# Performance work log

Measured on AMD Instinct MI355X. Metric: run time of the kernel, lower is better.

Reference implementation:

```python
import jax, jax.numpy as jnp
import numpy as np

B, S, D = 4, 4096, 2048
DQ = D // 4          # router hidden
DF = 4 * D           # layer_fn FFN hidden
CAPACITY = 0.125


def setup_inputs() -> dict:
    key = jax.random.key(0)
    ks = jax.random.split(key, 5)
    sc = 0.02
    return {
        "x":   jax.random.normal(ks[0], (B, S, D), jnp.float32),
        "Wr1": jax.random.normal(ks[1], (D, DQ), jnp.float32) * sc,
        "br1": jnp.zeros((DQ,), jnp.float32),
        "Wr2": jax.random.normal(ks[2], (DQ, 1), jnp.float32) * sc,
        "br2": jnp.zeros((1,), jnp.float32),
        "Wf1": jax.random.normal(ks[3], (D, DF), jnp.float32) * sc,
        "bf1": jnp.zeros((DF,), jnp.float32),
        "Wf2": jax.random.normal(ks[4], (DF, D), jnp.float32) * sc,
        "bf2": jnp.zeros((D,), jnp.float32),
    }


def reference(x, Wr1, br1, Wr2, br2, Wf1, bf1, Wf2, bf2):
    b, s, d = x.shape
    k = max(1, int(CAPACITY * s))

    # router: Linear -> ReLU -> Linear -> squeeze(-1)
    h = jax.nn.relu(jnp.einsum("bsd,dq->bsq", x, Wr1) + br1)
    scores = (jnp.einsum("bsq,qo->bso", h, Wr2) + br2)[..., 0]   # [B, S]

    # top-k token selection per batch row
    topk_scores, topk_idx = jax.lax.top_k(scores, k)             # [B, k]

    # gather selected tokens
    sel = jnp.take_along_axis(x, topk_idx[..., None], axis=1)    # [B, k, D]

    # layer_fn: standard FFN (D -> 4D -> D) on selected tokens only
    proc = jnp.einsum("bkf,fd->bkd",
                      jax.nn.relu(jnp.einsum("bkd,df->bkf", sel, Wf1) + bf1),
                      Wf2) + bf2                                 # [B, k, D]

    # scatter processed tokens back into a copy of x
    batch_idx = jnp.arange(b)[:, None]                           # [B, 1]
    output = x.at[batch_idx, topk_idx].set(proc)                 # [B, S, D]

    mask = jnp.zeros((b, s), dtype=bool).at[batch_idx, topk_idx].set(True)
    return output, mask
```

## Files before the change

kernel.cpp:

```cpp
#include <hip/hip_runtime.h>

#define B_    4
#define S_    4096
#define D_    2048
#define DQ_   512
#define DF_   8192
#define KSEL_ 512
#define M_    (B_ * S_)
#define MS_   (B_ * KSEL_)

typedef __attribute__((ext_vector_type(8))) short bf16x8;
typedef __attribute__((ext_vector_type(4))) float f32x4;
typedef __attribute__((address_space(3))) void as3_void;
typedef const __attribute__((address_space(1))) void as1_cvoid;

__device__ __forceinline__ unsigned short f2bf(float f) {
    unsigned u = __float_as_uint(f);
    u += 0x7FFFu + ((u >> 16) & 1u);
    return (unsigned short)(u >> 16);
}
__device__ __forceinline__ float bf2f(unsigned short h) {
    return __uint_as_float(((unsigned)h) << 16);
}

__device__ __forceinline__ void gload16(const void* g, void* l) {
    __builtin_amdgcn_global_load_lds((as1_cvoid*)g, (as3_void*)l, 16, 0, 0);
}

__global__ void split_copy_kernel(const float* __restrict__ x,
                                  unsigned short* __restrict__ xh,
                                  unsigned short* __restrict__ xl,
                                  float* __restrict__ out, int n8) {
    int i = blockIdx.x * blockDim.x + threadIdx.x;
    int stride = gridDim.x * blockDim.x;
    for (; i < n8; i += stride) {
        float4 a = ((const float4*)x)[2 * i];
        float4 b = ((const float4*)x)[2 * i + 1];
        ((float4*)out)[2 * i]     = a;
        ((float4*)out)[2 * i + 1] = b;
        float v[8] = {a.x, a.y, a.z, a.w, b.x, b.y, b.z, b.w};
        unsigned short hi[8], lo[8];
#pragma unroll
        for (int j = 0; j < 8; j++) {
            hi[j] = f2bf(v[j]);
            lo[j] = f2bf(v[j] - bf2f(hi[j]));
        }
        *(uint4*)(xh + (size_t)i * 8) = *(const uint4*)hi;
        *(uint4*)(xl + (size_t)i * 8) = *(const uint4*)lo;
    }
}

__global__ void wsplit_kernel(const float* __restrict__ W,
                              unsigned short* __restrict__ whiT,
                              unsigned short* __restrict__ wloT) {
    __shared__ float tile[32][33];
    int tx = threadIdx.x, ty = threadIdx.y;
    int n0 = blockIdx.x * 32, k0 = blockIdx.y * 32;
#pragma unroll
    for (int j = 0; j < 4; j++)
        tile[ty + j * 8][tx] = W[(size_t)(k0 + ty + j * 8) * DQ_ + n0 + tx];
    __syncthreads();
#pragma unroll
    for (int j = 0; j < 4; j++) {
        float v = tile[tx][ty + j * 8];
        unsigned short hi = f2bf(v);
        unsigned short lo = f2bf(v - bf2f(hi));
        size_t row = (size_t)(n0 + ty + j * 8) * D_;
        whiT[row + k0 + tx] = hi;
        wloT[row + k0 + tx] = lo;
    }
}

__global__ void transpose_bf16_kernel(const float* __restrict__ in,
                                      unsigned short* __restrict__ out,
                                      int R, int C) {
    __shared__ float tile[32][33];
    int tx = threadIdx.x, ty = threadIdx.y;
    int c0 = blockIdx.x * 32, r0 = blockIdx.y * 32;
#pragma unroll
    for (int j = 0; j < 4; j++)
        tile[ty + j * 8][tx] = in[(size_t)(r0 + ty + j * 8) * C + c0 + tx];
    __syncthreads();
#pragma unroll
    for (int j = 0; j < 4; j++)
        out[(size_t)(c0 + ty + j * 8) * R + r0 + tx] = f2bf(tile[tx][ty + j * 8]);
}

#define RSTAGE(bufp, ktX) do {                                              \
    const size_t ko_ = (size_t)(ktX) * 32;                                  \
    char* laH_ = (char*)(&sA[bufp][0][0]) + w * 1024;                       \
    char* laL_ = (char*)(&sA[bufp][1][0]) + w * 1024;                       \
    char* lbH_ = (char*)(&sB[bufp][0][0]) + w * 1024;                       \
    char* lbL_ = (char*)(&sB[bufp][1][0]) + w * 1024;                       \
    gload16(gAh + ko_,            laH_);                                    \
    gload16(gAh + 64 * D_ + ko_,  laH_ + 4096);                             \
    gload16(gAl + ko_,            laL_);                                    \
    gload16(gAl + 64 * D_ + ko_,  laL_ + 4096);                             \
    gload16(gBh + ko_,            lbH_);                                    \
    gload16(gBh + 64 * D_ + ko_,  lbH_ + 4096);                             \
    gload16(gBl + ko_,            lbL_);                                    \
    gload16(gBl + 64 * D_ + ko_,  lbL_ + 4096);                             \
  } while (0)

__global__ __launch_bounds__(256) void router_mfma(const unsigned short* __restrict__ xh,
                                                   const unsigned short* __restrict__ xl,
                                                   const unsigned short* __restrict__ whiT,
                                                   const unsigned short* __restrict__ wloT,
                                                   const float* __restrict__ br1,
                                                   const float* __restrict__ Wr2,
                                                   float* __restrict__ pscore) {
    __shared__ unsigned short sA[2][2][128 * 32];
    __shared__ unsigned short sB[2][2][128 * 32];
    const int t = threadIdx.x;
    const int w = t >> 6, l = t & 63;
    const int m0 = blockIdx.x * 128, n0 = blockIdx.y * 128;
    const int wr = w >> 1, wc = w & 1;

    f32x4 acc[4][4];
    const f32x4 zz = {0.f, 0.f, 0.f, 0.f};
#pragma unroll
    for (int m = 0; m < 4; m++)
#pragma unroll
        for (int n = 0; n < 4; n++) acc[m][n] = zz;

    const int srow = t >> 2;
    const int sch8 = (((t & 3) ^ ((t >> 3) & 3)) * 8);
    const unsigned short* gAh = xh + (size_t)(m0 + srow) * D_ + sch8;
    const unsigned short* gAl = xl + (size_t)(m0 + srow) * D_ + sch8;
    const unsigned short* gBh = whiT + (size_t)(n0 + srow) * D_ + sch8;
    const unsigned short* gBl = wloT + (size_t)(n0 + srow) * D_ + sch8;

    RSTAGE(0, 0);
    RSTAGE(1, 1);

    const int fro = ((l >> 4) ^ ((l >> 1) & 3)) * 8;
    const int arB = (wr * 64 + (l & 15)) * 32 + fro;
    const int brB = (wc * 64 + (l & 15)) * 32 + fro;

    for (int kt = 0; kt < 64; ++kt) {
        if (kt + 1 < 64) { asm volatile("s_waitcnt vmcnt(8)" ::: "memory"); }
        else             { asm volatile("s_waitcnt vmcnt(0)" ::: "memory"); }
        __builtin_amdgcn_s_barrier();
        __builtin_amdgcn_sched_barrier(0);
        const int cur = kt & 1;
        const unsigned short* LAh = &sA[cur][0][0];
        const unsigned short* LAl = &sA[cur][1][0];
        const unsigned short* LBh = &sB[cur][0][0];
        const unsigned short* LBl = &sB[cur][1][0];
        bf16x8 ah[4], al[4], bh[4], bl[4];
#pragma unroll
        for (int f = 0; f < 4; f++) ah[f] = *(const bf16x8*)(LAh + arB + f * 512);
#pragma unroll
        for (int f = 0; f < 4; f++) bh[f] = *(const bf16x8*)(LBh + brB + f * 512);
#pragma unroll
        for (int f = 0; f < 4; f++) bl[f] = *(const bf16x8*)(LBl + brB + f * 512);
#pragma unroll
        for (int f = 0; f < 4; f++) al[f] = *(const bf16x8*)(LAl + arB + f * 512);
        __builtin_amdgcn_s_setprio(1);
#pragma unroll
        for (int m = 0; m < 4; m++)
#pragma unroll
            for (int n = 0; n < 4; n++)
                acc[m][n] = __builtin_amdgcn_mfma_f32_16x16x32_bf16(ah[m], bh[n], acc[m][n], 0, 0, 0);
#pragma unroll
        for (int m = 0; m < 4; m++)
#pragma unroll
            for (int n = 0; n < 4; n++)
                acc[m][n] = __builtin_amdgcn_mfma_f32_16x16x32_bf16(ah[m], bl[n], acc[m][n], 0, 0, 0);
#pragma unroll
        for (int m = 0; m < 4; m++)
#pragma unroll
            for (int n = 0; n < 4; n++)
                acc[m][n] = __builtin_amdgcn_mfma_f32_16x16x32_bf16(al[m], bh[n], acc[m][n], 0, 0, 0);
        __builtin_amdgcn_s_setprio(0);
        __builtin_amdgcn_sched_barrier(0);
        __builtin_amdgcn_s_barrier();
        if (kt + 2 < 64) RSTAGE(cur, kt + 2);
    }

    float br1v[4], wr2v[4];
#pragma unroll
    for (int nf = 0; nf < 4; nf++) {
        int col = n0 + wc * 64 + nf * 16 + (l & 15);
        br1v[nf] = br1[col];
        wr2v[nf] = Wr2[col];
    }
#pragma unroll
    for (int mf = 0; mf < 4; mf++)
#pragma unroll
        for (int q = 0; q < 4; q++) {
            float s = 0.f;
#pragma unroll
            for (int nf = 0; nf < 4; nf++)
                s += fmaxf(acc[mf][nf][q] + br1v[nf], 0.f) * wr2v[nf];
#pragma unroll
            for (int off = 8; off >= 1; off >>= 1)
                s += __shfl_xor(s, off);
            if ((l & 15) == 0) {
                int row = m0 + wr * 64 + mf * 16 + (l >> 4) * 4 + q;
                pscore[(size_t)(blockIdx.y * 2 + wc) * M_ + row] = s;
            }
        }
}

__global__ __launch_bounds__(1024) void topk_kernel(const float* __restrict__ pscore,
                                                    const float* __restrict__ br2,
                                                    int* __restrict__ sel_idx,
                                                    float* __restrict__ maskF) {
    __shared__ unsigned long long keys[S_];
    __shared__ unsigned char flags[S_];
    int b = blockIdx.x, t = threadIdx.x;
    float bb = br2[0];
    for (int i = t; i < S_; i += 1024) {
        int m = b * S_ + i;
        float f = bb;
#pragma unroll
        for (int s8 = 0; s8 < 8; s8++) f += pscore[(size_t)s8 * M_ + m];
        unsigned u = __float_as_uint(f);
        u = (u & 0x80000000u) ? ~u : (u | 0x80000000u);
        keys[i] = ((unsigned long long)u << 32) | (unsigned)(S_ - 1 - i);
        flags[i] = 0;
    }
    __syncthreads();
    for (int k = 2; k <= S_; k <<= 1)
        for (int j = k >> 1; j > 0; j >>= 1) {
            for (int i = t; i < S_; i += 1024) {
                int l = i ^ j;
                if (l > i) {
                    unsigned long long a = keys[i], c = keys[l];
                    bool up = ((i & k) == 0);
                    if (up ? (a > c) : (a < c)) { keys[i] = c; keys[l] = a; }
                }
            }
            __syncthreads();
        }
    for (int i = t; i < KSEL_; i += 1024) {
        unsigned long long kk = keys[S_ - KSEL_ + i];
        int s = (S_ - 1) - (int)(kk & 0xFFFFFFFFu);
        sel_idx[b * KSEL_ + i] = s;
        flags[s] = 1;
    }
    __syncthreads();
    for (int i = t; i < S_; i += 1024)
        maskF[b * S_ + i] = flags[i] ? 1.0f : 0.0f;
}

__global__ void gather_kernel(const float* __restrict__ x, const int* __restrict__ sel_idx,
                              unsigned short* __restrict__ sel) {
    int jrow = blockIdx.x;
    int b = jrow >> 9;
    int tok = sel_idx[jrow];
    const float* src = x + ((size_t)(b * S_ + tok)) * D_;
    int t = threadIdx.x;
    float4 v0 = ((const float4*)src)[2 * t];
    float4 v1 = ((const float4*)src)[2 * t + 1];
    unsigned p0 = (unsigned)f2bf(v0.x) | ((unsigned)f2bf(v0.y) << 16);
    unsigned p1 = (unsigned)f2bf(v0.z) | ((unsigned)f2bf(v0.w) << 16);
    unsigned p2 = (unsigned)f2bf(v1.x) | ((unsigned)f2bf(v1.y) << 16);
    unsigned p3 = (unsigned)f2bf(v1.z) | ((unsigned)f2bf(v1.w) << 16);
    *(uint4*)(sel + (size_t)jrow * D_ + t * 8) = make_uint4(p0, p1, p2, p3);
}

#define STAGEAB(bufp, ktX) do {                                                   \
    const unsigned short* a_ = gA + (size_t)(ktX) * 64;                           \
    const unsigned short* b_ = gB + (size_t)(ktX) * 64;                           \
    char* la_ = (char*)(&lds[bufp][0][0]) + w * 1024;                             \
    char* lb_ = (char*)(&lds[bufp][1][0]) + w * 1024;                             \
    gload16(a_,                      la_);                                        \
    gload16(a_ +  64 * (size_t)K,    la_ + 8192);                                 \
    gload16(a_ + 128 * (size_t)K,    la_ + 16384);                                \
    gload16(a_ + 192 * (size_t)K,    la_ + 24576);                                \
    gload16(b_,                      lb_);                                        \
    gload16(b_ +  64 * (size_t)K,    lb_ + 8192);                                 \
    gload16(b_ + 128 * (size_t)K,    lb_ + 16384);                                \
    gload16(b_ + 192 * (size_t)K,    lb_ + 24576);                                \
  } while (0)

__global__ __launch_bounds__(512) void mfma_gemm256(const unsigned short* __restrict__ A,
                                                    const unsigned short* __restrict__ Bt,
                                                    int M, int N, int K, int kspan,
                                                    const float* __restrict__ bias,
                                                    unsigned short* __restrict__ Cbf,
                                                    float* __restrict__ partial,
                                                    int epi) {
    __shared__ unsigned short lds[2][2][256 * 64];
    const int t = threadIdx.x;
    const int w = t >> 6, l = t & 63;
    const int m0 = blockIdx.y * 256, n0 = blockIdx.x * 256;
    const int wr = w >> 2, wc = w & 3;
    const int kbeg = blockIdx.z * kspan;
    const int NT = kspan / 64;

    f32x4 acc[8][4];
    const f32x4 zz = {0.f, 0.f, 0.f, 0.f};
#pragma unroll
    for (int m = 0; m < 8; m++)
#pragma unroll
        for (int n = 0; n < 4; n++) acc[m][n] = zz;

    const int srow = t >> 3;
    const int sch8 = (((t & 7) ^ ((t >> 3) & 7)) * 8);
    const unsigned short* gA = A + (size_t)(m0 + srow) * K + kbeg + sch8;
    const unsigned short* gB = Bt + (size_t)(n0 + srow) * K + kbeg + sch8;

    STAGEAB(0, 0);
    STAGEAB(1, 1);

    for (int kt = 0; kt < NT; ++kt) {
        if (kt + 1 < NT) { asm volatile("s_waitcnt vmcnt(8)" ::: "memory"); }
        else             { asm volatile("s_waitcnt vmcnt(0)" ::: "memory"); }
        __builtin_amdgcn_s_barrier();
        __builtin_amdgcn_sched_barrier(0);
        const int cur = kt & 1;
        const unsigned short* LA = &lds[cur][0][0];
        const unsigned short* LB = &lds[cur][1][0];
#pragma unroll
        for (int kk = 0; kk < 2; kk++) {
            const int sw_ = ((kk * 4 + (l >> 4)) ^ (l & 7)) * 8;
            bf16x8 bfr[4], af0[4], af1[4];
#pragma unroll
            for (int n = 0; n < 4; n++)
                bfr[n] = *(const bf16x8*)(LB + (wc * 64 + n * 16 + (l & 15)) * 64 + sw_);
#pragma unroll
            for (int m = 0; m < 4; m++) {
                af0[m] = *(const bf16x8*)(LA + (wr * 128 + m * 16 + (l & 15)) * 64 + sw_);
                af1[m] = *(const bf16x8*)(LA + (wr * 128 + 64 + m * 16 + (l & 15)) * 64 + sw_);
            }
            __builtin_amdgcn_s_setprio(1);
#pragma unroll
            for (int m = 0; m < 4; m++)
#pragma unroll
                for (int n = 0; n < 4; n++)
                    acc[m][n] = __builtin_amdgcn_mfma_f32_16x16x32_bf16(af0[m], bfr[n], acc[m][n], 0, 0, 0);
#pragma unroll
            for (int m = 0; m < 4; m++)
#pragma unroll
                for (int n = 0; n < 4; n++)
                    acc[4 + m][n] = __builtin_amdgcn_mfma_f32_16x16x32_bf16(af1[m], bfr[n], acc[4 + m][n], 0, 0, 0);
            __builtin_amdgcn_s_setprio(0);
        }
        __builtin_amdgcn_sched_barrier(0);
        __builtin_amdgcn_s_barrier();
        if (kt + 2 < NT) STAGEAB(cur, kt + 2);
    }

    if (epi == 0) {
#pragma unroll
        for (int m = 0; m < 8; m++) {
            int rowb = m0 + wr * 128 + m * 16 + (l >> 4) * 4;
#pragma unroll
            for (int n = 0; n < 4; n++) {
                int col = n0 + wc * 64 + n * 16 + (l & 15);
                float bv = bias[col];
#pragma unroll
                for (int q = 0; q < 4; q++) {
                    float v = fmaxf(acc[m][n][q] + bv, 0.f);
                    Cbf[(size_t)(rowb + q) * N + col] = f2bf(v);
                }
            }
        }
    } else {
        float* pseg = partial + (size_t)blockIdx.z * M * N;
#pragma unroll
        for (int m = 0; m < 8; m++) {
            int rowb = m0 + wr * 128 + m * 16 + (l >> 4) * 4;
#pragma unroll
            for (int n = 0; n < 4; n++) {
                int col = n0 + wc * 64 + n * 16 + (l & 15);
#pragma unroll
                for (int q = 0; q < 4; q++)
                    pseg[(size_t)(rowb + q) * N + col] = acc[m][n][q];
            }
        }
    }
}

__global__ void reduce_scatter_kernel(const float* __restrict__ partial,
                                      const float* __restrict__ bias,
                                      const int* __restrict__ sel_idx,
                                      float* __restrict__ out) {
    int m = blockIdx.x;
    int t = threadIdx.x;
    int brow = m >> 9;
    int tok = sel_idx[m];
    float* orow = out + ((size_t)(brow * S_ + tok)) * D_;
    const float* p0 = partial + (size_t)m * D_;
    const size_t seg = (size_t)MS_ * D_;
#pragma unroll
    for (int r = 0; r < 2; r++) {
        int c = (t + r * 256) * 4;
        float4 v0 = *(const float4*)(p0 + c);
        float4 v1 = *(const float4*)(p0 + seg + c);
        float4 v2 = *(const float4*)(p0 + 2 * seg + c);
        float4 v3 = *(const float4*)(p0 + 3 * seg + c);
        float4 bv = *(const float4*)(bias + c);
        float4 o;
        o.x = v0.x + v1.x + v2.x + v3.x + bv.x;
        o.y = v0.y + v1.y + v2.y + v3.y + bv.y;
        o.z = v0.z + v1.z + v2.z + v3.z + bv.z;
        o.w = v0.w + v1.w + v2.w + v3.w + bv.w;
        *(float4*)(orow + c) = o;
    }
}

extern "C" void kernel_launch(void* const* d_in, const int* in_sizes, int n_in,
                              void* d_out, int out_size, void* d_ws, size_t ws_size,
                              hipStream_t stream) {
    const float* x   = (const float*)d_in[0];
    const float* Wr1 = (const float*)d_in[1];
    const float* br1 = (const float*)d_in[2];
    const float* Wr2 = (const float*)d_in[3];
    const float* br2 = (const float*)d_in[4];
    const float* Wf1 = (const float*)d_in[5];
    const float* bf1 = (const float*)d_in[6];
    const float* Wf2 = (const float*)d_in[7];
    const float* bf2 = (const float*)d_in[8];
    float* out = (float*)d_out;
    char* ws = (char*)d_ws;

    unsigned short* xh   = (unsigned short*)(ws);
    unsigned short* xl   = (unsigned short*)(ws + (64u << 20));
    unsigned short* whiT = (unsigned short*)(ws + (160u << 20));
    unsigned short* wloT = (unsigned short*)(ws + (162u << 20));
    float* pscore        = (float*)(ws + (168u << 20));
    int* sel_idx         = (int*)(ws + (169u << 20));
    float* partial       = (float*)(ws);
    unsigned short* w1t  = (unsigned short*)(ws + (64u << 20));
    unsigned short* w2t  = (unsigned short*)(ws + (96u << 20));
    unsigned short* h1   = (unsigned short*)(ws + (128u << 20));
    unsigned short* sel  = (unsigned short*)(ws + (160u << 20));
    float* maskF         = out + (size_t)B_ * S_ * D_;

    (void)in_sizes; (void)n_in; (void)out_size; (void)ws_size;

    split_copy_kernel<<<2048, 256, 0, stream>>>(x, xh, xl, out, (M_ * D_) / 8);
    wsplit_kernel<<<dim3(DQ_ / 32, D_ / 32), dim3(32, 8), 0, stream>>>(Wr1, whiT, wloT);
    router_mfma<<<dim3(M_ / 128, DQ_ / 128), 256, 0, stream>>>(
        xh, xl, whiT, wloT, br1, Wr2, pscore);
    topk_kernel<<<B_, 1024, 0, stream>>>(pscore, br2, sel_idx, maskF);
    gather_kernel<<<MS_, 256, 0, stream>>>(x, sel_idx, sel);
    transpose_bf16_kernel<<<dim3(DF_ / 32, D_ / 32), dim3(32, 8), 0, stream>>>(Wf1, w1t, D_, DF_);
    transpose_bf16_kernel<<<dim3(D_ / 32, DF_ / 32), dim3(32, 8), 0, stream>>>(Wf2, w2t, DF_, D_);
    mfma_gemm256<<<dim3(DF_ / 256, MS_ / 256, 1), 512, 0, stream>>>(
        sel, w1t, MS_, DF_, D_, D_, bf1, h1, nullptr, 0);
    mfma_gemm256<<<dim3(D_ / 256, MS_ / 256, 4), 512, 0, stream>>>(
        h1, w2t, MS_, D_, DF_, DF_ / 4, nullptr, nullptr, partial, 1);
    reduce_scatter_kernel<<<MS_, 256, 0, stream>>>(partial, bf2, sel_idx, out);
}
```

Baseline: 441.9 us.

## Replace full bitonic top-k with histogram radix select; store split-K partials as bf16

The top-k kernel now builds a 4096-bin histogram of the high bits of the score keys, finds the threshold bin with a suffix scan, and bitonic-sorts only the candidates in that bin instead of sorting all 4096 keys. The selected indices are written in token order rather than score order, which the scatter and mask outputs tolerate. The second FFN GEMM now writes its split-K partial sums as bf16 instead of fp32, halving partial-buffer traffic, and the reduce kernel reads bf16. This costs some extra rounding error in the output, and the atomic-based compaction makes candidate order nondeterministic.

```diff
diff --git a/kernel.cpp b/kernel.cpp
--- a/kernel.cpp
+++ b/kernel.cpp
@@ -207,42 +207,99 @@
                                                     const float* __restrict__ br2,
                                                     int* __restrict__ sel_idx,
                                                     float* __restrict__ maskF) {
-    __shared__ unsigned long long keys[S_];
+    __shared__ unsigned hist[4096];
+    __shared__ unsigned long long cand[4096];
     __shared__ unsigned char flags[S_];
+    __shared__ unsigned cnts[2];
+    __shared__ unsigned s_thr, s_above;
     int b = blockIdx.x, t = threadIdx.x;
     float bb = br2[0];
-    for (int i = t; i < S_; i += 1024) {
-        int m = b * S_ + i;
+
+    for (int i = t; i < 4096; i += 1024) { hist[i] = 0; flags[i] = 0; }
+    if (t < 2) cnts[t] = 0;
+    __syncthreads();
+
+    unsigned ureg[4];
+#pragma unroll
+    for (int r = 0; r < 4; r++) {
+        int i = t + r * 1024;
         float f = bb;
 #pragma unroll
-        for (int s8 = 0; s8 < 8; s8++) f += pscore[(size_t)s8 * M_ + m];
+        for (int s8 = 0; s8 < 8; s8++) f += pscore[(size_t)s8 * M_ + b * S_ + i];
         unsigned u = __float_as_uint(f);
         u = (u & 0x80000000u) ? ~u : (u | 0x80000000u);
-        keys[i] = ((unsigned long long)u << 32) | (unsigned)(S_ - 1 - i);
-        flags[i] = 0;
-    }
-    __syncthreads();
-    for (int k = 2; k <= S_; k <<= 1)
-        for (int j = k >> 1; j > 0; j >>= 1) {
-            for (int i = t; i < S_; i += 1024) {
-                int l = i ^ j;
-                if (l > i) {
-                    unsigned long long a = keys[i], c = keys[l];
+        ureg[r] = u;
+        atomicAdd(&hist[u >> 20], 1u);
+    }
+    __syncthreads();
+
+    for (int d = 1; d < 4096; d <<= 1) {
+        unsigned tmp[4];
+#pragma unroll
+        for (int r = 0; r < 4; r++) {
+            int i = t + r * 1024;
+            tmp[r] = (i + d < 4096) ? hist[i + d] : 0u;
+        }
+        __syncthreads();
+#pragma unroll
+        for (int r = 0; r < 4; r++) hist[t + r * 1024] += tmp[r];
+        __syncthreads();
+    }
+#pragma unroll
+    for (int r = 0; r < 4; r++) {
+        int i = t + r * 1024;
+        unsigned Si = hist[i];
+        unsigned Sn = (i + 1 < 4096) ? hist[i + 1] : 0u;
+        if (Si >= KSEL_ && Sn < KSEL_) { s_thr = (unsigned)i; s_above = Sn; }
+    }
+    __syncthreads();
+    const unsigned thr = s_thr;
+    const unsigned need = KSEL_ - s_above;
+
+#pragma unroll
+    for (int r = 0; r < 4; r++) {
+        int i = t + r * 1024;
+        unsigned u = ureg[r];
+        unsigned bin = u >> 20;
+        if (bin > thr) flags[i] = 1;
+        else if (bin == thr) {
+            unsigned slot = atomicAdd(&cnts[0], 1u);
+            cand[slot] = ((unsigned long long)u << 32) | (unsigned)(S_ - 1 - i);
+        }
+    }
+    __syncthreads();
+
+    unsigned nc = cnts[0];
+    unsigned ncp2 = 1; while (ncp2 < nc) ncp2 <<= 1;
+    for (unsigned i = t + nc; i < ncp2; i += 1024) cand[i] = 0ull;
+    __syncthreads();
+    for (unsigned k = 2; k <= ncp2; k <<= 1)
+        for (unsigned j = k >> 1; j > 0; j >>= 1) {
+            for (unsigned i = t; i < ncp2; i += 1024) {
+                unsigned li = i ^ j;
+                if (li > i) {
+                    unsigned long long a = cand[i], c = cand[li];
                     bool up = ((i & k) == 0);
-                    if (up ? (a > c) : (a < c)) { keys[i] = c; keys[l] = a; }
+                    if (up ? (a > c) : (a < c)) { cand[i] = c; cand[li] = a; }
                 }
             }
             __syncthreads();
         }
-    for (int i = t; i < KSEL_; i += 1024) {
-        unsigned long long kk = keys[S_ - KSEL_ + i];
-        int s = (S_ - 1) - (int)(kk & 0xFFFFFFFFu);
-        sel_idx[b * KSEL_ + i] = s;
-        flags[s] = 1;
-    }
-    __syncthreads();
-    for (int i = t; i < S_; i += 1024)
+    for (unsigned i = t; i < need; i += 1024) {
+        unsigned long long kk = cand[ncp2 - need + i];
+        flags[(S_ - 1) - (int)(kk & 0xFFFFFFFFu)] = 1;
+    }
+    __syncthreads();
+
+#pragma unroll
+    for (int r = 0; r < 4; r++) {
+        int i = t + r * 1024;
+        if (flags[i]) {
+            unsigned slot = atomicAdd(&cnts[1], 1u);
+            sel_idx[b * KSEL_ + slot] = i;
+        }
         maskF[b * S_ + i] = flags[i] ? 1.0f : 0.0f;
+    }
 }
 
 __global__ void gather_kernel(const float* __restrict__ x, const int* __restrict__ sel_idx,
@@ -281,7 +338,7 @@
                                                     int M, int N, int K, int kspan,
                                                     const float* __restrict__ bias,
                                                     unsigned short* __restrict__ Cbf,
-                                                    float* __restrict__ partial,
+                                                    unsigned short* __restrict__ partialB,
                                                     int epi) {
     __shared__ unsigned short lds[2][2][256 * 64];
     const int t = threadIdx.x;
@@ -360,7 +417,7 @@
             }
         }
     } else {
-        float* pseg = partial + (size_t)blockIdx.z * M * N;
+        unsigned short* pseg = partialB + (size_t)blockIdx.z * M * N;
 #pragma unroll
         for (int m = 0; m < 8; m++) {
             int rowb = m0 + wr * 128 + m * 16 + (l >> 4) * 4;
@@ -369,13 +426,13 @@
                 int col = n0 + wc * 64 + n * 16 + (l & 15);
 #pragma unroll
                 for (int q = 0; q < 4; q++)
-                    pseg[(size_t)(rowb + q) * N + col] = acc[m][n][q];
+                    pseg[(size_t)(rowb + q) * N + col] = f2bf(acc[m][n][q]);
             }
         }
     }
 }
 
-__global__ void reduce_scatter_kernel(const float* __restrict__ partial,
+__global__ void reduce_scatter_kernel(const unsigned short* __restrict__ partial,
                                       const float* __restrict__ bias,
                                       const int* __restrict__ sel_idx,
                                       float* __restrict__ out) {
@@ -384,23 +441,21 @@
     int brow = m >> 9;
     int tok = sel_idx[m];
     float* orow = out + ((size_t)(brow * S_ + tok)) * D_;
-    const float* p0 = partial + (size_t)m * D_;
+    int c = t * 8;
     const size_t seg = (size_t)MS_ * D_;
-#pragma unroll
-    for (int r = 0; r < 2; r++) {
-        int c = (t + r * 256) * 4;
-        float4 v0 = *(const float4*)(p0 + c);
-        float4 v1 = *(const float4*)(p0 + seg + c);
-        float4 v2 = *(const float4*)(p0 + 2 * seg + c);
-        float4 v3 = *(const float4*)(p0 + 3 * seg + c);
-        float4 bv = *(const float4*)(bias + c);
-        float4 o;
-        o.x = v0.x + v1.x + v2.x + v3.x + bv.x;
-        o.y = v0.y + v1.y + v2.y + v3.y + bv.y;
-        o.z = v0.z + v1.z + v2.z + v3.z + bv.z;
-        o.w = v0.w + v1.w + v2.w + v3.w + bv.w;
-        *(float4*)(orow + c) = o;
-    }
+    const unsigned short* pb = partial + (size_t)m * D_ + c;
+    float o[8];
+#pragma unroll
+    for (int j = 0; j < 8; j++) o[j] = bias[c + j];
+#pragma unroll
+    for (int s = 0; s < 4; s++) {
+        uint4 v = *(const uint4*)(pb + s * seg);
+        const unsigned short* e = (const unsigned short*)&v;
+#pragma unroll
+        for (int j = 0; j < 8; j++) o[j] += bf2f(e[j]);
+    }
+    *(float4*)(orow + c)     = *(float4*)&o[0];
+    *(float4*)(orow + c + 4) = *(float4*)&o[4];
 }
 
 extern "C" void kernel_launch(void* const* d_in, const int* in_sizes, int n_in,
@@ -418,18 +473,18 @@
     float* out = (float*)d_out;
     char* ws = (char*)d_ws;
 
-    unsigned short* xh   = (unsigned short*)(ws);
-    unsigned short* xl   = (unsigned short*)(ws + (64u << 20));
-    unsigned short* whiT = (unsigned short*)(ws + (160u << 20));
-    unsigned short* wloT = (unsigned short*)(ws + (162u << 20));
-    float* pscore        = (float*)(ws + (168u << 20));
-    int* sel_idx         = (int*)(ws + (169u << 20));
-    float* partial       = (float*)(ws);
-    unsigned short* w1t  = (unsigned short*)(ws + (64u << 20));
-    unsigned short* w2t  = (unsigned short*)(ws + (96u << 20));
-    unsigned short* h1   = (unsigned short*)(ws + (128u << 20));
-    unsigned short* sel  = (unsigned short*)(ws + (160u << 20));
-    float* maskF         = out + (size_t)B_ * S_ * D_;
+    unsigned short* xh    = (unsigned short*)(ws);
+    unsigned short* xl    = (unsigned short*)(ws + (64u << 20));
+    unsigned short* whiT  = (unsigned short*)(ws + (160u << 20));
+    unsigned short* wloT  = (unsigned short*)(ws + (162u << 20));
+    float* pscore         = (float*)(ws + (168u << 20));
+    int* sel_idx          = (int*)(ws + (169u << 20));
+    unsigned short* partB = (unsigned short*)(ws);
+    unsigned short* w1t   = (unsigned short*)(ws + (64u << 20));
+    unsigned short* w2t   = (unsigned short*)(ws + (96u << 20));
+    unsigned short* h1    = (unsigned short*)(ws + (128u << 20));
+    unsigned short* sel   = (unsigned short*)(ws + (160u << 20));
+    float* maskF          = out + (size_t)B_ * S_ * D_;
 
     (void)in_sizes; (void)n_in; (void)out_size; (void)ws_size;
 
@@ -444,6 +499,6 @@
     mfma_gemm256<<<dim3(DF_ / 256, MS_ / 256, 1), 512, 0, stream>>>(
         sel, w1t, MS_, DF_, D_, D_, bf1, h1, nullptr, 0);
     mfma_gemm256<<<dim3(D_ / 256, MS_ / 256, 4), 512, 0, stream>>>(
-        h1, w2t, MS_, D_, DF_, DF_ / 4, nullptr, nullptr, partial, 1);
-    reduce_scatter_kernel<<<MS_, 256, 0, stream>>>(partial, bf2, sel_idx, out);
-}
+        h1, w2t, MS_, D_, DF_, DF_ / 4, nullptr, nullptr, partB, 1);
+    reduce_scatter_kernel<<<MS_, 256, 0, stream>>>(partB, bf2, sel_idx, out);
+}
```

Measured after the change: 386.1 us, median of 3. 12.6% less time.
